# Optimization experiments

Measured on AMD Instinct MI355X. Metric: run time of the kernel, lower is better.

## Reference

```python
import jax, jax.numpy as jnp
import numpy as np

RESOLUTIONS = [33, 65, 129, 257, 513]
BAL = 0.5
K_CONFLICT = 3  # fixed unrolled conflict-resolution passes per level


def _up2(x):
    """Exact 2x-1 bilinear upsample with align_corners=True. [H,W]->[2H-1,2W-1]."""
    H, W = x.shape
    y = jnp.zeros((2 * H - 1, W), x.dtype)
    y = y.at[::2].set(x).at[1::2].set(0.5 * (x[:-1] + x[1:]))
    z = jnp.zeros((2 * H - 1, 2 * W - 1), x.dtype)
    z = z.at[:, ::2].set(y).at[:, 1::2].set(0.5 * (y[:, :-1] + y[:, 1:]))
    return z


def _any3x3(mask):
    """3x3 'smooth conv > 0' == any neighbor true. bool [H,W] -> bool [H,W]."""
    x = mask.astype(jnp.float32)[None, None]
    k = jnp.ones((1, 1, 3, 3), jnp.float32)
    y = jax.lax.conv_general_dilated(x, k, (1, 1), ((1, 1), (1, 1)))
    return y[0, 0] > 0


def setup_inputs() -> dict:
    key = jax.random.key(0)
    ks = jax.random.split(key, 4)
    d = 128
    return {
        "W1": jax.random.normal(ks[0], (2, d), jnp.float32) * 1.0,
        "b1": jnp.zeros((d,), jnp.float32),
        "W2": jax.random.normal(ks[1], (d, d), jnp.float32) / np.sqrt(d),
        "b2": jnp.zeros((d,), jnp.float32),
        "W3": jax.random.normal(ks[2], (d, 1), jnp.float32) * (2.0 / np.sqrt(d)),
        "b3": jnp.zeros((1,), jnp.float32),
        "b_min": jnp.zeros((2,), jnp.float32),
        "b_max": jnp.ones((2,), jnp.float32),
    }


def reference(W1, b1, W2, b2, W3, b3, b_min, b_max):
    def eval_grid(H, W):
        # align_corners=True: grid coords / (res-1) in [0,1], identical at every level
        u = jnp.linspace(0.0, 1.0, W, dtype=jnp.float32)
        v = jnp.linspace(0.0, 1.0, H, dtype=jnp.float32)
        X, Y = jnp.meshgrid(u, v)          # [H,W] each
        pts = jnp.stack([X, Y], -1).reshape(-1, 2)
        pts = b_min + pts * (b_max - b_min)
        h = jnp.tanh(pts @ W1 + b1)
        h = jnp.tanh(h @ W2 + b2)
        return jax.nn.sigmoid(h @ W3 + b3).reshape(H, W)

    Rf = RESOLUTIONS[-1]
    R0 = RESOLUTIONS[0]
    occ = eval_grid(R0, R0)                       # level-0 full evaluation
    calc = jnp.zeros((Rf, Rf), bool)
    s0 = (Rf - 1) // (R0 - 1)
    calc = calc.at[::s0, ::s0].set(True)

    for R in RESOLUTIONS[1:]:
        s = (Rf - 1) // (R - 1)
        occ_i = _up2(occ)                          # bilinear interp, align_corners=True
        valid = _up2((occ > BAL).astype(occ.dtype))
        boundary = (valid > 0) & (valid < 1)       # crossing band
        boundary = _any3x3(boundary)               # smooth_conv3x3 > 0
        calc_lvl = calc[::s, ::s]
        boundary = boundary & ~calc_lvl            # exclude already-evaluated points
        q = eval_grid(R, R)                        # query_func on level grid (masked use)
        conflicts = boundary & ((occ_i - BAL) * (q - BAL) < 0)
        occ = jnp.where(boundary, q, occ_i)        # scatter query values at boundary
        calc_lvl = calc_lvl | boundary
        # conflict resolution: re-evaluate 8-neighborhood of conflicting points
        for _ in range(K_CONFLICT):
            cand = _any3x3(conflicts) & ~calc_lvl
            conflicts = cand & ((occ - BAL) * (q - BAL) < 0)
            occ = jnp.where(cand, q, occ)
            calc_lvl = calc_lvl | cand
        calc = calc.at[::s, ::s].set(calc_lvl)

    return occ[None, None]                         # [1, 1, Rf, Rf]
```

## Files before the change

kernel.cpp:

```cpp
#include <hip/hip_runtime.h>

typedef unsigned char u8;
typedef float f32x4 __attribute__((ext_vector_type(4)));
typedef _Float16 f16x8 __attribute__((ext_vector_type(8)));

#define DIM 128
#define TM  128

__device__ __forceinline__ float fast_tanh(float x) {
    float e = __builtin_amdgcn_exp2f(x * 2.885390081777927f);
    return 1.0f - 2.0f * __builtin_amdgcn_rcpf(e + 1.0f);
}
__device__ __forceinline__ float fast_sigmoid(float x) {
    float e = __builtin_amdgcn_exp2f(x * -1.4426950408889634f);
    return __builtin_amdgcn_rcpf(1.0f + e);
}

__global__ __launch_bounds__(256, 4) void eval_q4(
    const float* __restrict__ W1, const float* __restrict__ b1,
    const float* __restrict__ W2, const float* __restrict__ b2,
    const float* __restrict__ W3, const float* __restrict__ b3,
    const float* __restrict__ bmin, const float* __restrict__ bmax,
    float* __restrict__ q4)
{
    __shared__ __align__(16) _Float16 sW2T[DIM * DIM];

    const int R = 513;
    const int N = R * R;
    const int tid = threadIdx.x;
    const int m0 = blockIdx.x * TM;

    #pragma unroll
    for (int s = 0; s < 8; ++s) {
        int chunk = s * 256 + tid;
        int n = chunk & 127, ko = chunk >> 7;
        f16x8 v;
        #pragma unroll
        for (int qq = 0; qq < 8; ++qq)
            v[qq] = (_Float16)W2[(ko * 8 + qq) * DIM + n];
        int slot = ko ^ (n & 15);
        *(f16x8*)&sW2T[n * DIM + slot * 8] = v;
    }

    const int w = tid >> 6, lane = tid & 63;
    const int l15 = lane & 15, lg = lane >> 4;

    const float inv = 1.0f / 512.0f;
    const float bx0 = bmin[0], by0 = bmin[1];
    const float sx = bmax[0] - bx0, sy = bmax[1] - by0;
    float xs[2], ys[2];
    #pragma unroll
    for (int mf = 0; mf < 2; ++mf) {
        int pi = m0 + w * 32 + mf * 16 + l15;
        int pg = (pi < N) ? pi : N - 1;
        int gi = pg / R, gj = pg - gi * R;
        xs[mf] = bx0 + (float)gj * inv * sx;
        ys[mf] = by0 + (float)gi * inv * sy;
    }

    f32x4 acc[2][8];
    #pragma unroll
    for (int nf = 0; nf < 8; ++nf) {
        float b2v = b2[nf * 16 + l15];
        acc[0][nf] = (f32x4)(b2v);
        acc[1][nf] = (f32x4)(b2v);
    }

    __syncthreads();

    #pragma unroll
    for (int kf = 0; kf < 4; ++kf) {
        const int kbase = kf * 32 + lg * 8;
        f16x8 bh[8];
        #pragma unroll
        for (int nf = 0; nf < 8; ++nf) {
            int c = nf * 16 + l15;
            int slot = (kf * 4 + lg) ^ l15;
            bh[nf] = *(const f16x8*)&sW2T[c * DIM + slot * 8];
        }
        f32x4 wxa = *(const f32x4*)&W1[kbase];
        f32x4 wxb = *(const f32x4*)&W1[kbase + 4];
        f32x4 wya = *(const f32x4*)&W1[DIM + kbase];
        f32x4 wyb = *(const f32x4*)&W1[DIM + kbase + 4];
        f32x4 b1a = *(const f32x4*)&b1[kbase];
        f32x4 b1b = *(const f32x4*)&b1[kbase + 4];
        f16x8 ah[2];
        #pragma unroll
        for (int mf = 0; mf < 2; ++mf) {
            float x = xs[mf], y = ys[mf];
            #pragma unroll
            for (int qq = 0; qq < 4; ++qq)
                ah[mf][qq] = (_Float16)fast_tanh(fmaf(x, wxa[qq], fmaf(y, wya[qq], b1a[qq])));
            #pragma unroll
            for (int qq = 0; qq < 4; ++qq)
                ah[mf][4 + qq] = (_Float16)fast_tanh(fmaf(x, wxb[qq], fmaf(y, wyb[qq], b1b[qq])));
        }
        #pragma unroll
        for (int nf = 0; nf < 8; ++nf)
            #pragma unroll
            for (int mf = 0; mf < 2; ++mf)
                acc[mf][nf] = __builtin_amdgcn_mfma_f32_16x16x32_f16(ah[mf], bh[nf], acc[mf][nf], 0, 0, 0);
    }

    float rs[2][4] = {{0,0,0,0},{0,0,0,0}};
    #pragma unroll
    for (int nf = 0; nf < 8; ++nf) {
        float w3v = W3[nf * 16 + l15];
        #pragma unroll
        for (int mf = 0; mf < 2; ++mf)
            #pragma unroll
            for (int rg = 0; rg < 4; ++rg)
                rs[mf][rg] += fast_tanh(acc[mf][nf][rg]) * w3v;
    }
    #pragma unroll
    for (int mf = 0; mf < 2; ++mf)
        #pragma unroll
        for (int rg = 0; rg < 4; ++rg) {
            float v = rs[mf][rg];
            v += __shfl_xor(v, 1);
            v += __shfl_xor(v, 2);
            v += __shfl_xor(v, 4);
            v += __shfl_xor(v, 8);
            rs[mf][rg] = v;
        }
    if (l15 == 0) {
        float b3v = b3[0];
        #pragma unroll
        for (int mf = 0; mf < 2; ++mf)
            #pragma unroll
            for (int rg = 0; rg < 4; ++rg) {
                int po = m0 + w * 32 + mf * 16 + lg * 4 + rg;
                if (po < N) q4[po] = fast_sigmoid(rs[mf][rg] + b3v);
            }
    }
}

template<int TS, int NT>
__global__ __launch_bounds__(NT) void level_kernel(
    const float* __restrict__ occP, int opRow, int opCol,
    const u8* __restrict__ calcP, int Rp,
    const float* __restrict__ q4, int qRow, int qCol,
    float* __restrict__ occOut, u8* __restrict__ calcOut, int R)
{
    constexpr int HW = TS + 8;
    __shared__ u8 sRaw[HW * HW], sCfA[HW * HW], sCfB[HW * HW];
    const int nT = (R + TS - 1) / TS;
    const int bi = blockIdx.x / nT, bj = blockIdx.x - bi * nT;
    const int fi0 = bi * TS - 4, fj0 = bj * TS - 4;
    const int c = threadIdx.x;
    const int li = c / HW, lj = c - li * HW;
    const int fi = fi0 + li, fj = fj0 + lj;
    const bool inG = (fi >= 0 && fi < R && fj >= 0 && fj < R);
    const float BAL = 0.5f;

    float occ = 0.5f, qv = 0.5f;
    u8 rw = 0; bool cal = false;
    if (inG) qv = q4[fi * qRow + fj * qCol];
    if (inG) {
        int ip = fi >> 1, jp = fj >> 1;
        float tl = occP[ip * opRow + jp * opCol];
        int oi = fi & 1, oj = fj & 1;
        bool b;
        if (!oi && !oj) { occ = tl; b = false; }
        else if (oi && !oj) {
            float bl = occP[(ip + 1) * opRow + jp * opCol];
            occ = 0.5f * (tl + bl);
            b = (tl > BAL) != (bl > BAL);
        } else if (!oi && oj) {
            float tr = occP[ip * opRow + (jp + 1) * opCol];
            occ = 0.5f * (tl + tr);
            b = (tl > BAL) != (tr > BAL);
        } else {
            float bl = occP[(ip + 1) * opRow + jp * opCol];
            float tr = occP[ip * opRow + (jp + 1) * opCol];
            float br = occP[(ip + 1) * opRow + (jp + 1) * opCol];
            occ = 0.5f * (0.5f * (tl + bl) + 0.5f * (tr + br));
            bool m0 = tl > BAL, m1 = bl > BAL, m2 = tr > BAL, m3 = br > BAL;
            b = (m0 | m1 | m2 | m3) && !(m0 & m1 & m2 & m3);
        }
        rw = b ? 1 : 0;
        if (((fi | fj) & 1) == 0) cal = calcP ? (calcP[ip * Rp + jp] != 0) : true;
    }
    sRaw[c] = rw; sCfA[c] = 0; sCfB[c] = 0;

    if (__syncthreads_or(rw)) {
        u8 cf = 0;
        if (li >= 1 && li < HW - 1 && lj >= 1 && lj < HW - 1 && inG) {
            bool b = false;
            #pragma unroll
            for (int di = -1; di <= 1; ++di)
                #pragma unroll
                for (int dj = -1; dj <= 1; ++dj)
                    if (sRaw[(li + di) * HW + (lj + dj)]) b = true;
            b = b && !cal;
            cf = (b && (occ - BAL) * (qv - BAL) < 0.0f) ? 1 : 0;
            if (b) { occ = qv; cal = true; }
            sCfA[c] = cf;
        }
        int haveCf = __syncthreads_or((int)cf);

        #pragma unroll
        for (int it = 0; it < 3; ++it) {
            if (!haveCf) break;
            const u8* cin = (it & 1) ? sCfB : sCfA;
            u8* cout      = (it & 1) ? sCfA : sCfB;
            int lo = 2 + it, hi = HW - 2 - it;
            u8 nc = 0;
            if (li >= lo && li < hi && lj >= lo && lj < hi && inG) {
                bool any = false;
                #pragma unroll
                for (int di = -1; di <= 1; ++di)
                    #pragma unroll
                    for (int dj = -1; dj <= 1; ++dj)
                        if (cin[(li + di) * HW + (lj + dj)]) any = true;
                bool cand = any && !cal;
                nc = (cand && (occ - BAL) * (qv - BAL) < 0.0f) ? 1 : 0;
                if (cand) { occ = qv; cal = true; }
                cout[c] = nc;
            }
            haveCf = __syncthreads_or((int)nc);
        }
    }

    if (li >= 4 && li < HW - 4 && lj >= 4 && lj < HW - 4 && inG) {
        occOut[fi * R + fj] = occ;
        calcOut[fi * R + fj] = cal ? 1 : 0;
    }
}

extern "C" void kernel_launch(void* const* d_in, const int* in_sizes, int n_in,
                              void* d_out, int out_size, void* d_ws, size_t ws_size,
                              hipStream_t stream) {
    const float* W1   = (const float*)d_in[0];
    const float* b1   = (const float*)d_in[1];
    const float* W2   = (const float*)d_in[2];
    const float* b2   = (const float*)d_in[3];
    const float* W3   = (const float*)d_in[4];
    const float* b3   = (const float*)d_in[5];
    const float* bmin = (const float*)d_in[6];
    const float* bmax = (const float*)d_in[7];

    const int RF = 513, N513 = RF * RF;

    float* q4   = (float*)d_ws;
    float* occA = q4 + N513;
    float* occB = occA + N513;
    u8* calcA = (u8*)(occB + N513);
    u8* calcB = calcA + N513;
    float* out = (float*)d_out;

    eval_q4<<<(N513 + TM - 1) / TM, 256, 0, stream>>>(
        W1, b1, W2, b2, W3, b3, bmin, bmax, q4);

    level_kernel<8, 256><<<81, 256, 0, stream>>>(
        q4, RF * 16, 16, (const u8*)nullptr, 33,
        q4, RF * 8, 8, occA, calcB, 65);
    level_kernel<16, 576><<<81, 576, 0, stream>>>(
        occA, 65, 1, calcB, 65,
        q4, RF * 4, 4, occB, calcA, 129);
    level_kernel<16, 576><<<289, 576, 0, stream>>>(
        occB, 129, 1, calcA, 129,
        q4, RF * 2, 2, occA, calcB, 257);
    level_kernel<16, 576><<<1089, 576, 0, stream>>>(
        occA, 257, 1, calcB, 257,
        q4, RF, 1, out, calcA, 513);
}
```

Baseline: 50.27 us.

## Evaluate MLP densely only at 257 grid, sparsely on 513 tiles near boundary

Instead of evaluating the MLP on all 513x513 points up front, the dense evaluation now covers only the 257x257 grid, which supplies coarser levels by strided sampling. A new eval_fine kernel runs after level 257 and tests each 16x16 tile of the fine grid, plus a 4-point halo, for a crossing band derived from the level-257 occupancy. It evaluates the MLP only for tiles that need it and exits early otherwise. This removes most of the dense fine-grid MLP work, at the cost of an extra kernel and serialising fine evaluation after the coarse levels. Skipped tiles leave q4 unwritten, which is safe only if the final level never reads q4 there.

```diff
diff --git a/kernel.cpp b/kernel.cpp
--- a/kernel.cpp
+++ b/kernel.cpp
@@ -16,20 +16,8 @@
     return __builtin_amdgcn_rcpf(1.0f + e);
 }
 
-__global__ __launch_bounds__(256, 4) void eval_q4(
-    const float* __restrict__ W1, const float* __restrict__ b1,
-    const float* __restrict__ W2, const float* __restrict__ b2,
-    const float* __restrict__ W3, const float* __restrict__ b3,
-    const float* __restrict__ bmin, const float* __restrict__ bmax,
-    float* __restrict__ q4)
-{
-    __shared__ __align__(16) _Float16 sW2T[DIM * DIM];
-
-    const int R = 513;
-    const int N = R * R;
-    const int tid = threadIdx.x;
-    const int m0 = blockIdx.x * TM;
-
+__device__ __forceinline__ void stage_w2(const float* __restrict__ W2,
+                                         _Float16* sW2T, int tid) {
     #pragma unroll
     for (int s = 0; s < 8; ++s) {
         int chunk = s * 256 + tid;
@@ -41,23 +29,14 @@
         int slot = ko ^ (n & 15);
         *(f16x8*)&sW2T[n * DIM + slot * 8] = v;
     }
-
-    const int w = tid >> 6, lane = tid & 63;
-    const int l15 = lane & 15, lg = lane >> 4;
-
-    const float inv = 1.0f / 512.0f;
-    const float bx0 = bmin[0], by0 = bmin[1];
-    const float sx = bmax[0] - bx0, sy = bmax[1] - by0;
-    float xs[2], ys[2];
-    #pragma unroll
-    for (int mf = 0; mf < 2; ++mf) {
-        int pi = m0 + w * 32 + mf * 16 + l15;
-        int pg = (pi < N) ? pi : N - 1;
-        int gi = pg / R, gj = pg - gi * R;
-        xs[mf] = bx0 + (float)gj * inv * sx;
-        ys[mf] = by0 + (float)gi * inv * sy;
-    }
-
+}
+
+__device__ __forceinline__ void mlp_wave(
+    const float xs[2], const float ys[2], const _Float16* sW2T,
+    const float* __restrict__ W1, const float* __restrict__ b1,
+    const float* __restrict__ b2, const float* __restrict__ W3,
+    int lg, int l15, float rs[2][4])
+{
     f32x4 acc[2][8];
     #pragma unroll
     for (int nf = 0; nf < 8; ++nf) {
@@ -65,18 +44,15 @@
         acc[0][nf] = (f32x4)(b2v);
         acc[1][nf] = (f32x4)(b2v);
     }
-
-    __syncthreads();
-
     #pragma unroll
     for (int kf = 0; kf < 4; ++kf) {
         const int kbase = kf * 32 + lg * 8;
         f16x8 bh[8];
         #pragma unroll
         for (int nf = 0; nf < 8; ++nf) {
-            int c = nf * 16 + l15;
+            int cc = nf * 16 + l15;
             int slot = (kf * 4 + lg) ^ l15;
-            bh[nf] = *(const f16x8*)&sW2T[c * DIM + slot * 8];
+            bh[nf] = *(const f16x8*)&sW2T[cc * DIM + slot * 8];
         }
         f32x4 wxa = *(const f32x4*)&W1[kbase];
         f32x4 wxb = *(const f32x4*)&W1[kbase + 4];
@@ -101,8 +77,10 @@
             for (int mf = 0; mf < 2; ++mf)
                 acc[mf][nf] = __builtin_amdgcn_mfma_f32_16x16x32_f16(ah[mf], bh[nf], acc[mf][nf], 0, 0, 0);
     }
-
-    float rs[2][4] = {{0,0,0,0},{0,0,0,0}};
+    #pragma unroll
+    for (int mf = 0; mf < 2; ++mf)
+        #pragma unroll
+        for (int rg = 0; rg < 4; ++rg) rs[mf][rg] = 0.0f;
     #pragma unroll
     for (int nf = 0; nf < 8; ++nf) {
         float w3v = W3[nf * 16 + l15];
@@ -123,6 +101,40 @@
             v += __shfl_xor(v, 8);
             rs[mf][rg] = v;
         }
+}
+
+__global__ __launch_bounds__(256, 4) void eval_grid(
+    const float* __restrict__ W1, const float* __restrict__ b1,
+    const float* __restrict__ W2, const float* __restrict__ b2,
+    const float* __restrict__ W3, const float* __restrict__ b3,
+    const float* __restrict__ bmin, const float* __restrict__ bmax,
+    float* __restrict__ out, int R)
+{
+    __shared__ __align__(16) _Float16 sW2T[DIM * DIM];
+    const int N = R * R;
+    const int tid = threadIdx.x;
+    const int m0 = blockIdx.x * TM;
+    stage_w2(W2, sW2T, tid);
+
+    const int w = tid >> 6, lane = tid & 63;
+    const int l15 = lane & 15, lg = lane >> 4;
+
+    const float inv = 1.0f / (float)(R - 1);
+    const float bx0 = bmin[0], by0 = bmin[1];
+    const float sx = bmax[0] - bx0, sy = bmax[1] - by0;
+    float xs[2], ys[2];
+    #pragma unroll
+    for (int mf = 0; mf < 2; ++mf) {
+        int pi = m0 + w * 32 + mf * 16 + l15;
+        int pg = (pi < N) ? pi : N - 1;
+        int gi = pg / R, gj = pg - gi * R;
+        xs[mf] = bx0 + (float)gj * inv * sx;
+        ys[mf] = by0 + (float)gi * inv * sy;
+    }
+    __syncthreads();
+
+    float rs[2][4];
+    mlp_wave(xs, ys, sW2T, W1, b1, b2, W3, lg, l15, rs);
     if (l15 == 0) {
         float b3v = b3[0];
         #pragma unroll
@@ -130,8 +142,82 @@
             #pragma unroll
             for (int rg = 0; rg < 4; ++rg) {
                 int po = m0 + w * 32 + mf * 16 + lg * 4 + rg;
-                if (po < N) q4[po] = fast_sigmoid(rs[mf][rg] + b3v);
+                if (po < N) out[po] = fast_sigmoid(rs[mf][rg] + b3v);
             }
+    }
+}
+
+__global__ __launch_bounds__(256, 4) void eval_fine(
+    const float* __restrict__ W1, const float* __restrict__ b1,
+    const float* __restrict__ W2, const float* __restrict__ b2,
+    const float* __restrict__ W3, const float* __restrict__ b3,
+    const float* __restrict__ bmin, const float* __restrict__ bmax,
+    const float* __restrict__ occ3, float* __restrict__ q4)
+{
+    __shared__ __align__(16) _Float16 sW2T[DIM * DIM];
+    const int bi = blockIdx.x / 33, bj = blockIdx.x - bi * 33;
+    const int ti0 = bi * 16, tj0 = bj * 16;
+    const int tid = threadIdx.x;
+
+    bool need = false;
+    for (int s = tid; s < 576; s += 256) {
+        int li = s / 24, lj = s - li * 24;
+        int fi = ti0 - 4 + li, fj = tj0 - 4 + lj;
+        if (fi >= 0 && fi < 513 && fj >= 0 && fj < 513) {
+            int oi = fi & 1, oj = fj & 1;
+            if (oi | oj) {
+                int ip = fi >> 1, jp = fj >> 1;
+                bool m0 = occ3[ip * 257 + jp] > 0.5f;
+                bool b;
+                if (oi && !oj)      b = m0 != (occ3[(ip + 1) * 257 + jp] > 0.5f);
+                else if (!oi && oj) b = m0 != (occ3[ip * 257 + jp + 1] > 0.5f);
+                else {
+                    bool m1 = occ3[(ip + 1) * 257 + jp] > 0.5f;
+                    bool m2 = occ3[ip * 257 + jp + 1] > 0.5f;
+                    bool m3 = occ3[(ip + 1) * 257 + jp + 1] > 0.5f;
+                    b = (m0 | m1 | m2 | m3) && !(m0 & m1 & m2 & m3);
+                }
+                need |= b;
+            }
+        }
+    }
+    if (!__syncthreads_or(need ? 1 : 0)) return;
+
+    stage_w2(W2, sW2T, tid);
+    __syncthreads();
+
+    const int w = tid >> 6, lane = tid & 63;
+    const int l15 = lane & 15, lg = lane >> 4;
+    const float inv = 1.0f / 512.0f;
+    const float bx0 = bmin[0], by0 = bmin[1];
+    const float sx = bmax[0] - bx0, sy = bmax[1] - by0;
+    const float b3v = b3[0];
+
+    #pragma unroll
+    for (int half = 0; half < 2; ++half) {
+        float xs[2], ys[2];
+        #pragma unroll
+        for (int mf = 0; mf < 2; ++mf) {
+            int p = half * 128 + w * 32 + mf * 16 + l15;
+            int gi = ti0 + (p >> 4), gj = tj0 + (p & 15);
+            if (gi > 512) gi = 512;
+            if (gj > 512) gj = 512;
+            xs[mf] = bx0 + (float)gj * inv * sx;
+            ys[mf] = by0 + (float)gi * inv * sy;
+        }
+        float rs[2][4];
+        mlp_wave(xs, ys, sW2T, W1, b1, b2, W3, lg, l15, rs);
+        if (l15 == 0) {
+            #pragma unroll
+            for (int mf = 0; mf < 2; ++mf)
+                #pragma unroll
+                for (int rg = 0; rg < 4; ++rg) {
+                    int p = half * 128 + w * 32 + mf * 16 + lg * 4 + rg;
+                    int gi = ti0 + (p >> 4), gj = tj0 + (p & 15);
+                    if (gi < 513 && gj < 513)
+                        q4[gi * 513 + gj] = fast_sigmoid(rs[mf][rg] + b3v);
+                }
+        }
     }
 }
 
@@ -240,28 +326,33 @@
     const float* bmin = (const float*)d_in[6];
     const float* bmax = (const float*)d_in[7];
 
-    const int RF = 513, N513 = RF * RF;
-
-    float* q4   = (float*)d_ws;
+    const int N513 = 513 * 513, N257 = 257 * 257;
+
+    float* q257 = (float*)d_ws;
+    float* q4   = q257 + N257;
     float* occA = q4 + N513;
     float* occB = occA + N513;
     u8* calcA = (u8*)(occB + N513);
     u8* calcB = calcA + N513;
     float* out = (float*)d_out;
 
-    eval_q4<<<(N513 + TM - 1) / TM, 256, 0, stream>>>(
-        W1, b1, W2, b2, W3, b3, bmin, bmax, q4);
+    eval_grid<<<(N257 + TM - 1) / TM, 256, 0, stream>>>(
+        W1, b1, W2, b2, W3, b3, bmin, bmax, q257, 257);
 
     level_kernel<8, 256><<<81, 256, 0, stream>>>(
-        q4, RF * 16, 16, (const u8*)nullptr, 33,
-        q4, RF * 8, 8, occA, calcB, 65);
+        q257, 257 * 8, 8, (const u8*)nullptr, 33,
+        q257, 257 * 4, 4, occA, calcB, 65);
     level_kernel<16, 576><<<81, 576, 0, stream>>>(
         occA, 65, 1, calcB, 65,
-        q4, RF * 4, 4, occB, calcA, 129);
+        q257, 257 * 2, 2, occB, calcA, 129);
     level_kernel<16, 576><<<289, 576, 0, stream>>>(
         occB, 129, 1, calcA, 129,
-        q4, RF * 2, 2, occA, calcB, 257);
+        q257, 257, 1, occA, calcB, 257);
+
+    eval_fine<<<1089, 256, 0, stream>>>(
+        W1, b1, W2, b2, W3, b3, bmin, bmax, occA, q4);
+
     level_kernel<16, 576><<<1089, 576, 0, stream>>>(
         occA, 257, 1, calcB, 257,
-        q4, RF, 1, out, calcA, 513);
-}
+        q4, 513, 1, out, calcA, 513);
+}
```

Measured after the change: 84.56 us. +68.2%, slower.
